# Kernel tuning notes

Hardware: AMD Instinct MI355X
Metric: run time of the kernel (lower is better)

Reference implementation:

```python
import jax, jax.numpy as jnp
import numpy as np
import math

IMAGE_SIZE = 256
N_ANGLES = 180


def setup_inputs() -> dict:
    key = jax.random.key(0)
    x = jax.random.normal(key, (4, 1, IMAGE_SIZE, IMAGE_SIZE), dtype=jnp.float32)
    return {"x": x}


def reference(x) -> jnp.ndarray:
    # Radon transform, circle=True: mask to inscribed circle, then for each
    # angle bilinearly sample the image along rotated coordinates
    # (torch.grid_sample, align_corners=True, zeros padding) and sum along rays.
    B = x.shape[0]
    S = IMAGE_SIZE
    A = N_ANGLES
    img = x.reshape(B, S, S)

    # circular mask (matches torch: sqrt(dist2) <= center with center = S//2)
    center = S // 2
    yy, xx = jnp.meshgrid(jnp.arange(S), jnp.arange(S), indexing='ij')
    dist = jnp.sqrt(((xx - center) ** 2 + (yy - center) ** 2).astype(jnp.float32))
    img = img * (dist <= center).astype(img.dtype)
    img_flat = img.reshape(B, S * S)

    # projection coordinates: meshgrid('ij') of linspace(-S/2, S/2, S)
    lin = jnp.linspace(-S / 2.0, S / 2.0, S, dtype=jnp.float32)
    X, Y = jnp.meshgrid(lin, lin, indexing='ij')  # [S,S]; X varies along i
    Xf, Yf = X.ravel(), Y.ravel()                 # [S*S]

    # all rotation angles at once: torch.linspace(0, 180, A) degrees
    ang = jnp.linspace(0.0, 180.0, A, dtype=jnp.float32) * (math.pi / 180.0)
    c = jnp.cos(ang)[:, None]  # [A,1]
    s = jnp.sin(ang)[:, None]
    half = S / 2.0
    gx = (c * Xf - s * Yf) / half  # [A, S*S], normalized grid x (width)
    gy = (s * Xf + c * Yf) / half  # [A, S*S], normalized grid y (height)

    # align_corners=True: pixel = (g + 1)/2 * (S - 1)
    px = (gx + 1.0) * 0.5 * (S - 1)
    py = (gy + 1.0) * 0.5 * (S - 1)

    x0 = jnp.floor(px)
    y0 = jnp.floor(py)
    wx = px - x0
    wy = py - y0
    x0i = x0.astype(jnp.int32)
    y0i = y0.astype(jnp.int32)
    x1i = x0i + 1
    y1i = y0i + 1

    def corner(xi, yi, w):
        # zeros padding: out-of-bounds corners contribute 0
        valid = (xi >= 0) & (xi < S) & (yi >= 0) & (yi < S)
        idx = jnp.clip(yi, 0, S - 1) * S + jnp.clip(xi, 0, S - 1)  # [A, S*S]
        vals = jnp.take(img_flat, idx, axis=1)                      # [B, A, S*S]
        return vals * (w * valid.astype(img.dtype))

    acc = (corner(x0i, y0i, (1.0 - wx) * (1.0 - wy))
           + corner(x1i, y0i, wx * (1.0 - wy))
           + corner(x0i, y1i, (1.0 - wx) * wy)
           + corner(x1i, y1i, wx * wy))  # [B, A, S*S]

    # flat order is (i, j) from meshgrid('ij'); torch sums over output H == i
    sinogram = acc.reshape(B, A, S, S).sum(axis=2)  # [B, A, S]
    return sinogram
```

## Files before the change

### kernel.cpp

```cpp
#include <hip/hip_runtime.h>
#include <hip/hip_fp16.h>
#include <math.h>

#define S 256
#define A 180
#define B 4
#define PMAX 296
#define NR 137

__global__ void radon_mask_f16(const float* __restrict__ in, __half* __restrict__ out,
                               float* __restrict__ osino) {
    int idx = blockIdx.x * 256 + threadIdx.x;
    int p = idx & (S * S - 1);
    int y = p >> 8;
    int x = p & 255;
    int dx = x - 128, dy = y - 128;
    float v = in[idx];
    v = (dx * dx + dy * dy <= 16384) ? v : 0.0f;
    out[idx] = __float2half(v);
    if (idx < A * B * S) osino[idx] = 0.0f;
}

__global__ __launch_bounds__(1024, 8) void radon_lds_kernel(const __half* __restrict__ img,
                                                            float* __restrict__ out) {
    __shared__ __half lds[NR * PMAX];

    const int a = blockIdx.x;
    const int b = blockIdx.y;
    const int h = blockIdx.z;
    const int tid = threadIdx.x;

    float ang = (float)a * (float)(M_PI / 179.0);
    float sn, cs;
    sincosf(ang, &sn, &cs);

    int P = 266;
    {
        float best = 1e9f;
        for (int cand = 266; cand <= PMAX; cand += 2) {
            float sd = 0.5f * fabsf((float)cand * cs - sn);
            float m = sd - 2.0f * floorf(sd * 0.5f);
            float score = fabsf(m - 1.0f);
            if (score < best) { best = score; P = cand; }
        }
    }
    const int Ph = P >> 1;
    const int row0 = h ? 124 : -4;

    uint* l32 = (uint*)lds;
    {
        int nz = NR * Ph;
#pragma unroll
        for (int k = 0; k < 20; ++k) {
            int p = k * 1024 + tid;
            if (p < nz) l32[p] = 0u;
        }
    }
    __syncthreads();
    {
        const int r0img = h ? 124 : 0;
        const uint* __restrict__ src = (const uint*)(img + (size_t)b * (S * S));
#pragma unroll
        for (int k = 0; k < 17; ++k) {
            int p = k * 1024 + tid;
            if (p < 132 * 128) {
                int r = p >> 7;
                int xd = p & 127;
                int dstrow = r + (h ? 0 : 4);
                l32[dstrow * Ph + xd + 2] = src[(r0img + r) * 128 + xd];
            }
        }
    }
    __syncthreads();

    const int j = tid >> 2;
    const int q = tid & 3;

    const float ry = (float)j - 127.5f;
    const float bx = fmaf(-sn, ry, 127.5f);
    const float by = fmaf(cs, ry, 127.5f);
    const float ry2 = ry * ry;

    float hd = sqrtf(16934.0f - ry2);
    int ilo = max((int)ceilf(127.5f - hd), 0);
    int ihi = min((int)floorf(127.5f + hd) + 1, S);

    float tsf = 127.5f + (128.0f - by) / sn;
    tsf = fminf(fmaxf(tsf, 0.0f), 256.0f);
    int isplit = (int)ceilf(tsf);
    int lo0 = h ? max(ilo, isplit) : ilo;
    int hi0 = h ? ihi : min(ihi, isplit);
    int len = max(hi0 - lo0, 0);
    int lo = lo0 + ((q * len) >> 2);
    int hi = lo0 + (((q + 1) * len) >> 2);

    const int base = -row0 * P + 4;

    float acc = 0.0f;

#pragma unroll 4
    for (int i = lo; i < hi; ++i) {
        float rx = (float)i - 127.5f;
        float px = fmaf(cs, rx, bx);
        float py = fmaf(sn, rx, by);

        float x0f = floorf(px);
        float y0f = floorf(py);
        float wx = px - x0f;
        float wy = py - y0f;
        int x0 = (int)x0f;
        int y0 = (int)y0f;
        float ux = 1.0f - wx;
        float uy = 1.0f - wy;
        float w00 = ux * uy;
        float w10 = wx * uy;
        float w01 = ux * wy;
        float w11 = wx * wy;

        const __half* p0 = &lds[base + y0 * P + x0];
        float v00 = __half2float(p0[0]);
        float v10 = __half2float(p0[1]);
        float v01 = __half2float(p0[P]);
        float v11 = __half2float(p0[P + 1]);

        acc = fmaf(w00, v00, fmaf(w10, v10, fmaf(w01, v01, fmaf(w11, v11, acc))));
    }

    __syncthreads();
    float* red = (float*)lds;
    red[tid] = acc;
    __syncthreads();
    if (tid < 256) {
        float4 v = ((const float4*)red)[tid];
        atomicAdd(&out[((size_t)b * A + a) * S + tid], v.x + v.y + v.z + v.w);
    }
}

extern "C" void kernel_launch(void* const* d_in, const int* in_sizes, int n_in,
                              void* d_out, int out_size, void* d_ws, size_t ws_size,
                              hipStream_t stream) {
    const float* x = (const float*)d_in[0];
    float* out = (float*)d_out;
    __half* masked = (__half*)d_ws;

    radon_mask_f16<<<dim3((B * S * S) / 256), dim3(256), 0, stream>>>(x, masked, out);
    radon_lds_kernel<<<dim3(A, B, 2), dim3(1024), 0, stream>>>(masked, out);
}
```

Before: 92.42 us.

## Split image into four row bands with pre-paired fp16 LDS layout and dot2

Each block now covers a 64-row band, so the grid has four bands in z instead of two halves. The band is stored in LDS twice as packed 32-bit half pairs, once aligned and once shifted by one pixel, so each bilinear sample takes two 32-bit LDS reads. The weights are packed to fp16 and accumulated with fdot2. This replaces the per-angle search for a conflict-avoiding pitch and the separate zero-fill pass, at the cost of twice the blocks, more per-block fixed overhead, and fp16-rounded weights.

Result: slower. 112.7 us (+22.0%).

```diff
diff --git a/kernel.cpp b/kernel.cpp
--- a/kernel.cpp
+++ b/kernel.cpp
@@ -5,8 +5,17 @@
 #define S 256
 #define A 180
 #define B 4
-#define PMAX 296
-#define NR 137
+#define RS 133
+#define NRW 73
+#define ARR (NRW * RS)
+
+typedef __fp16 h2 __attribute__((ext_vector_type(2)));
+
+#if defined(__has_builtin)
+#if __has_builtin(__builtin_amdgcn_fdot2)
+#define USE_DOT2 1
+#endif
+#endif
 
 __global__ void radon_mask_f16(const float* __restrict__ in, __half* __restrict__ out,
                                float* __restrict__ osino) {
@@ -23,51 +32,33 @@
 
 __global__ __launch_bounds__(1024, 8) void radon_lds_kernel(const __half* __restrict__ img,
                                                             float* __restrict__ out) {
-    __shared__ __half lds[NR * PMAX];
+    __shared__ uint lds_u[2 * ARR];
 
     const int a = blockIdx.x;
     const int b = blockIdx.y;
     const int h = blockIdx.z;
     const int tid = threadIdx.x;
+    const int ystart = 64 * h - 4;
 
     float ang = (float)a * (float)(M_PI / 179.0);
     float sn, cs;
     sincosf(ang, &sn, &cs);
 
-    int P = 266;
     {
-        float best = 1e9f;
-        for (int cand = 266; cand <= PMAX; cand += 2) {
-            float sd = 0.5f * fabsf((float)cand * cs - sn);
-            float m = sd - 2.0f * floorf(sd * 0.5f);
-            float score = fabsf(m - 1.0f);
-            if (score < best) { best = score; P = cand; }
-        }
-    }
-    const int Ph = P >> 1;
-    const int row0 = h ? 124 : -4;
-
-    uint* l32 = (uint*)lds;
-    {
-        int nz = NR * Ph;
-#pragma unroll
-        for (int k = 0; k < 20; ++k) {
-            int p = k * 1024 + tid;
-            if (p < nz) l32[p] = 0u;
-        }
-    }
-    __syncthreads();
-    {
-        const int r0img = h ? 124 : 0;
         const uint* __restrict__ src = (const uint*)(img + (size_t)b * (S * S));
 #pragma unroll
-        for (int k = 0; k < 17; ++k) {
-            int p = k * 1024 + tid;
-            if (p < 132 * 128) {
-                int r = p >> 7;
-                int xd = p & 127;
-                int dstrow = r + (h ? 0 : 4);
-                l32[dstrow * Ph + xd + 2] = src[(r0img + r) * 128 + xd];
+        for (int it = 0; it < 10; ++it) {
+            int p = it * 1024 + tid;
+            if (p < NRW * 131) {
+                int r = p / 131;
+                int ko = p - r * 131;
+                int kk = ko - 2;
+                int g = ystart + r;
+                bool gv = ((unsigned)g < 256u);
+                uint d0 = (gv && (unsigned)kk < 128u) ? src[g * 128 + kk] : 0u;
+                uint d1 = (gv && (unsigned)(kk + 1) < 128u) ? src[g * 128 + kk + 1] : 0u;
+                lds_u[r * RS + ko] = d0;
+                lds_u[ARR + r * RS + ko] = (d0 >> 16) | (d1 << 16);
             }
         }
     }
@@ -85,49 +76,67 @@
     int ilo = max((int)ceilf(127.5f - hd), 0);
     int ihi = min((int)floorf(127.5f + hd) + 1, S);
 
-    float tsf = 127.5f + (128.0f - by) / sn;
-    tsf = fminf(fmaxf(tsf, 0.0f), 256.0f);
-    int isplit = (int)ceilf(tsf);
-    int lo0 = h ? max(ilo, isplit) : ilo;
-    int hi0 = h ? ihi : min(ihi, isplit);
+    float invsn = 1.0f / sn;
+    bool neg = (sn < 0.0f);
+    float cLo = neg ? (float)(64 * h + 64) : (float)(64 * h);
+    float cHi = neg ? (float)(64 * h) : (float)(64 * h + 64);
+    float tLo = 127.5f + (cLo - by) * invsn;
+    float tHi = 127.5f + (cHi - by) * invsn;
+    int FLo = (int)fminf(fmaxf(ceilf(tLo), 0.0f), 256.0f);
+    int FHi = (int)fminf(fmaxf(ceilf(tHi), 0.0f), 256.0f);
+    bool openLo = (h == (neg ? 3 : 0));
+    bool openHi = (h == (neg ? 0 : 3));
+    int lo0 = openLo ? ilo : max(ilo, FLo);
+    int hi0 = openHi ? ihi : min(ihi, FHi);
     int len = max(hi0 - lo0, 0);
     int lo = lo0 + ((q * len) >> 2);
     int hi = lo0 + (((q + 1) * len) >> 2);
 
-    const int base = -row0 * P + 4;
+    const float bxp = fmaf(-127.5f, cs, bx);
+    const float byl = fmaf(-127.5f, sn, by) - (float)ystart;
 
-    float acc = 0.0f;
+    float acc0 = 0.0f, acc1 = 0.0f;
 
 #pragma unroll 4
     for (int i = lo; i < hi; ++i) {
-        float rx = (float)i - 127.5f;
-        float px = fmaf(cs, rx, bx);
-        float py = fmaf(sn, rx, by);
+        float fi = (float)i;
+        float px = fmaf(cs, fi, bxp);
+        float py = fmaf(sn, fi, byl);
 
         float x0f = floorf(px);
         float y0f = floorf(py);
         float wx = px - x0f;
         float wy = py - y0f;
         int x0 = (int)x0f;
-        int y0 = (int)y0f;
+        int yl = (int)y0f;
+        int k = x0 >> 1;
+        int par = x0 & 1;
+        int addr = yl * RS + (k + 2) + par * ARR;
+
+        uint d0 = lds_u[addr];
+        uint d1 = lds_u[addr + RS];
+
         float ux = 1.0f - wx;
         float uy = 1.0f - wy;
-        float w00 = ux * uy;
-        float w10 = wx * uy;
-        float w01 = ux * wy;
-        float w11 = wx * wy;
-
-        const __half* p0 = &lds[base + y0 * P + x0];
-        float v00 = __half2float(p0[0]);
-        float v10 = __half2float(p0[1]);
-        float v01 = __half2float(p0[P]);
-        float v11 = __half2float(p0[P + 1]);
-
-        acc = fmaf(w00, v00, fmaf(w10, v10, fmaf(w01, v01, fmaf(w11, v11, acc))));
+#ifdef USE_DOT2
+        h2 w0 = __builtin_amdgcn_cvt_pkrtz(ux * uy, wx * uy);
+        h2 w1 = __builtin_amdgcn_cvt_pkrtz(ux * wy, wx * wy);
+        acc0 = __builtin_amdgcn_fdot2(__builtin_bit_cast(h2, d0), w0, acc0, false);
+        acc1 = __builtin_amdgcn_fdot2(__builtin_bit_cast(h2, d1), w1, acc1, false);
+#else
+        float v00 = __half2float(__ushort_as_half((unsigned short)(d0 & 0xffffu)));
+        float v10 = __half2float(__ushort_as_half((unsigned short)(d0 >> 16)));
+        float v01 = __half2float(__ushort_as_half((unsigned short)(d1 & 0xffffu)));
+        float v11 = __half2float(__ushort_as_half((unsigned short)(d1 >> 16)));
+        acc0 = fmaf(ux * uy, v00, fmaf(wx * uy, v10, acc0));
+        acc1 = fmaf(ux * wy, v01, fmaf(wx * wy, v11, acc1));
+#endif
     }
 
+    float acc = acc0 + acc1;
+
     __syncthreads();
-    float* red = (float*)lds;
+    float* red = (float*)lds_u;
     red[tid] = acc;
     __syncthreads();
     if (tid < 256) {
@@ -144,5 +153,5 @@
     __half* masked = (__half*)d_ws;
 
     radon_mask_f16<<<dim3((B * S * S) / 256), dim3(256), 0, stream>>>(x, masked, out);
-    radon_lds_kernel<<<dim3(A, B, 2), dim3(1024), 0, stream>>>(masked, out);
+    radon_lds_kernel<<<dim3(A, B, 4), dim3(1024), 0, stream>>>(masked, out);
 }
```
